# Kernel optimization log

Measured on AMD Instinct MI355X. Metric: run time of the kernel, lower is better.

## Reference

```python
import jax, jax.numpy as jnp
import numpy as np

B, N, C, D, H, L, F = 64, 256, 16, 512, 8, 8, 2048
HD = D // H
PI = np.pi


def _ln(x, w, b, eps=1e-5):
    mu = jnp.mean(x, -1, keepdims=True)
    var = jnp.mean(jnp.square(x - mu), -1, keepdims=True)
    return (x - mu) * jax.lax.rsqrt(var + eps) * w + b


def _forward(x_node, x_full, Wp, bp, cls, e_w1, e_b1, e_w2, e_b2, edge_scale,
             qkv_w, qkv_b, out_w, out_b, ln1_w, ln1_b, ln2_w, ln2_b,
             ff1_w, ff1_b, ff2_w, ff2_b, cl_ln_w, cl_ln_b, cl_w1, cl_b1, cl_w2, cl_b2):
    Bq, Nq, _ = x_node.shape
    # pairwise kaon geometry from absolute y/phi
    y = x_full[:, :, 14]
    phi = x_full[:, :, 15]
    dy = jnp.abs(y[:, :, None] - y[:, None, :])                                  # [B,N,N]
    dphi = jnp.abs(jnp.mod(phi[:, :, None] - phi[:, None, :] + PI, 2 * PI) - PI)
    dr = jnp.sqrt(dy * dy + dphi * dphi + 1e-8)
    ef = jnp.stack([dy, dphi, dr], -1)                                           # [B,N,N,3]
    hmid = jax.nn.gelu(ef @ e_w1.T + e_b1, approximate=False)                    # [B,N,N,16]
    raw = hmid @ e_w2.T + e_b2                                                   # [B,N,N,H]
    central = jnp.mean(raw, axis=2).transpose(0, 2, 1)                           # [B,H,N]
    edge_bias = raw.transpose(0, 3, 1, 2)                                        # [B,H,N,N]
    bias = jnp.zeros((Bq, H, Nq + 1, Nq + 1), x_node.dtype)
    bias = bias.at[:, :, 1:, 1:].set(edge_bias)
    bias = bias.at[:, :, 0, 1:].set(central * edge_scale)
    bias = bias.at[:, :, 1:, 0].set(central * edge_scale)

    h = x_node @ Wp.T + bp
    h = jnp.concatenate([jnp.broadcast_to(cls, (Bq, 1, D)), h], axis=1)          # [B,S,D]
    S = Nq + 1
    scale = 1.0 / np.sqrt(HD)
    for l in range(L):  # pre-norm TransformerEncoderLayer (activation=relu, no final norm)
        x = _ln(h, ln1_w[l], ln1_b[l])
        qkv = x @ qkv_w[l].T + qkv_b[l]
        q, k, v = jnp.split(qkv, 3, axis=-1)
        q = q.reshape(Bq, S, H, HD).transpose(0, 2, 1, 3)
        k = k.reshape(Bq, S, H, HD).transpose(0, 2, 1, 3)
        v = v.reshape(Bq, S, H, HD).transpose(0, 2, 1, 3)
        scores = jnp.einsum('bhqd,bhkd->bhqk', q, k) * scale + bias
        attn = jax.nn.softmax(scores, axis=-1)
        o = jnp.einsum('bhqk,bhkd->bhqd', attn, v).transpose(0, 2, 1, 3).reshape(Bq, S, D)
        h = h + o @ out_w[l].T + out_b[l]
        x = _ln(h, ln2_w[l], ln2_b[l])
        h = h + jax.nn.relu(x @ ff1_w[l].T + ff1_b[l]) @ ff2_w[l].T + ff2_b[l]
    x = _ln(h[:, 0], cl_ln_w, cl_ln_b)
    return jax.nn.gelu(x @ cl_w1.T + cl_b1, approximate=False) @ cl_w2.T + cl_b2  # [B,2]


def setup_inputs() -> dict:
    key = jax.random.key(0)
    ks = iter(jax.random.split(key, 40))
    f32 = jnp.float32

    def nrm(shape, s=0.02):
        return (s * jax.random.normal(next(ks), shape)).astype(f32)

    return {
        'x_node': jax.random.normal(next(ks), (B, N, C), f32),
        'x_full': jax.random.normal(next(ks), (B, N, 16), f32),
        'Wp': nrm((D, C)), 'bp': jnp.zeros((D,), f32),
        'cls': nrm((1, 1, D)),
        'e_w1': nrm((16, 3), 0.3), 'e_b1': jnp.zeros((16,), f32),
        'e_w2': nrm((H, 16), 0.01), 'e_b2': jnp.zeros((H,), f32),
        'edge_scale': jnp.full((1,), 0.1, f32),
        'qkv_w': nrm((L, 3 * D, D)), 'qkv_b': jnp.zeros((L, 3 * D), f32),
        'out_w': nrm((L, D, D)), 'out_b': jnp.zeros((L, D), f32),
        'ln1_w': jnp.ones((L, D), f32), 'ln1_b': jnp.zeros((L, D), f32),
        'ln2_w': jnp.ones((L, D), f32), 'ln2_b': jnp.zeros((L, D), f32),
        'ff1_w': nrm((L, F, D)), 'ff1_b': jnp.zeros((L, F), f32),
        'ff2_w': nrm((L, D, F)), 'ff2_b': jnp.zeros((L, D), f32),
        'cl_ln_w': jnp.ones((D,), f32), 'cl_ln_b': jnp.zeros((D,), f32),
        'cl_w1': nrm((D // 2, D)), 'cl_b1': jnp.zeros((D // 2,), f32),
        'cl_w2': nrm((2, D // 2)), 'cl_b2': jnp.zeros((2,), f32),
    }


def reference(x_node, x_full, Wp, bp, cls, e_w1, e_b1, e_w2, e_b2, edge_scale,
              qkv_w, qkv_b, out_w, out_b, ln1_w, ln1_b, ln2_w, ln2_b,
              ff1_w, ff1_b, ff2_w, ff2_b, cl_ln_w, cl_ln_b, cl_w1, cl_b1, cl_w2, cl_b2):
    return _forward(x_node, x_full, Wp, bp, cls, e_w1, e_b1, e_w2, e_b2, edge_scale,
                    qkv_w, qkv_b, out_w, out_b, ln1_w, ln1_b, ln2_w, ln2_b,
                    ff1_w, ff1_b, ff2_w, ff2_b, cl_ln_w, cl_ln_b, cl_w1, cl_b1, cl_w2, cl_b2)
```

## Files before the change

kernel.cpp:

```cpp
#include <hip/hip_runtime.h>
#include <hip/hip_bf16.h>
#include <stdint.h>

#define PI_F     3.14159265358979323846f
#define TWO_PI_F 6.28318530717958647692f
#define INV2PI_F 0.15915494309189535f

typedef __attribute__((ext_vector_type(8))) short bf16x8;
typedef __attribute__((ext_vector_type(4))) float f32x4;

#define BB 64
#define NN 256
#define SS 257
#define DD 512
#define HH 8
#define HDD 64
#define LL 8
#define MTOK 16448
#define MPAD 16512
#define BSTR 264
#define VSTR 320

__device__ __forceinline__ float b2f(unsigned short u){
  union { float f; uint32_t i; } c; c.i = ((uint32_t)u) << 16; return c.f;
}
__device__ __forceinline__ unsigned short f2b(float f){
  union { float f; uint32_t i; } c; c.f = f;
  uint32_t r = c.i + 0x7FFFu + ((c.i >> 16) & 1u);
  return (unsigned short)(r >> 16);
}
__device__ __forceinline__ float gelu_fast(float z){
  const float z2 = z*z;
  const float u2 = z * (1.5957691216f + 0.071354816f*z2);
  const float e = __expf(u2);
  const float th = 1.f - 2.f/(1.f + e);
  return 0.5f*z*(1.f + th);
}

typedef __attribute__((address_space(1))) unsigned char ga_t;
typedef __attribute__((address_space(3))) unsigned char ls_t;
__device__ __forceinline__ void gl_lds16(const void* g, void* l){
  __builtin_amdgcn_global_load_lds((ga_t*)g, (ls_t*)l, 16, 0, 0);
}

__global__ __launch_bounds__(256) void cvt_kernel(const float* __restrict__ src,
                                                  unsigned short* __restrict__ dst, int n2){
  int i = blockIdx.x*256 + threadIdx.x;
  int stride = gridDim.x*256;
  for (; i < n2; i += stride){
    float2 v = ((const float2*)src)[i];
    ((uint32_t*)dst)[i] = (uint32_t)f2b(v.x) | ((uint32_t)f2b(v.y) << 16);
  }
}

__global__ __launch_bounds__(256) void edge_kernel(
    const float* __restrict__ x_full, const float* __restrict__ e_w1, const float* __restrict__ e_b1,
    const float* __restrict__ e_w2, const float* __restrict__ e_b2,
    unsigned short* __restrict__ bias, float* __restrict__ central)
{
  const int bi = blockIdx.x;
  const int b = bi >> 8, i = bi & 255;
  const int j = threadIdx.x;
  const float yi = x_full[((long)b*NN + i)*16 + 14];
  const float fi = x_full[((long)b*NN + i)*16 + 15];
  const float yj = x_full[((long)b*NN + j)*16 + 14];
  const float fj = x_full[((long)b*NN + j)*16 + 15];
  const float dy = fabsf(yi - yj);
  const float xw = fi - fj + PI_F;
  const float tw = xw * INV2PI_F;
  const float md = (tw - floorf(tw)) * TWO_PI_F;
  const float dphi = fabsf(md - PI_F);
  const float dr = sqrtf(dy*dy + dphi*dphi + 1e-8f);
  float raw[8];
  #pragma unroll
  for (int hh = 0; hh < 8; ++hh) raw[hh] = e_b2[hh];
  #pragma unroll
  for (int k = 0; k < 16; ++k){
    float z = e_w1[k*3]*dy + e_w1[k*3+1]*dphi + e_w1[k*3+2]*dr + e_b1[k];
    float g = gelu_fast(z);
    #pragma unroll
    for (int hh = 0; hh < 8; ++hh) raw[hh] += g * e_w2[hh*16 + k];
  }
  #pragma unroll
  for (int hh = 0; hh < 8; ++hh)
    bias[(((long)b*HH + hh)*SS + 1 + i)*BSTR + 1 + j] = f2b(raw[hh]);
  #pragma unroll
  for (int m = 1; m < 64; m <<= 1)
    #pragma unroll
    for (int hh = 0; hh < 8; ++hh) raw[hh] += __shfl_xor(raw[hh], m);
  __shared__ float cw[4][8];
  const int wv = j >> 6;
  if ((j & 63) == 0)
    for (int hh = 0; hh < 8; ++hh) cw[wv][hh] = raw[hh];
  __syncthreads();
  if (j < 8){
    float t = cw[0][j] + cw[1][j] + cw[2][j] + cw[3][j];
    central[((long)b*NN + i)*HH + j] = t * (1.f/NN);
  }
}

__global__ __launch_bounds__(256) void edge_border_kernel(
    const float* __restrict__ central, const float* __restrict__ edge_scale,
    unsigned short* __restrict__ bias)
{
  const int bh = blockIdx.x;
  const int b = bh >> 3, h = bh & 7;
  const int j = threadIdx.x;
  const float es = edge_scale[0];
  const float cv = central[((long)b*NN + j)*HH + h] * es;
  const long base = (long)bh*SS*BSTR;
  const unsigned short u = f2b(cv);
  bias[base + 1 + j] = u;
  bias[base + (long)(1+j)*BSTR] = u;
  if (j == 0) bias[base] = 0;
}

__global__ __launch_bounds__(256) void proj_kernel(
    const float* __restrict__ x_node, const float* __restrict__ Wp,
    const float* __restrict__ bp, const float* __restrict__ cls, float* __restrict__ hb)
{
  const int t = blockIdx.x;
  const int tid = threadIdx.x;
  const int b = t / SS, s2 = t - b*SS;
  float2 o;
  if (s2 == 0){
    o = *(const float2*)(cls + tid*2);
  } else {
    const float* xr = x_node + ((long)b*NN + (s2-1))*16;
    float xv[16];
    #pragma unroll
    for (int c2 = 0; c2 < 16; ++c2) xv[c2] = xr[c2];
    float oo[2];
    #pragma unroll
    for (int e = 0; e < 2; ++e){
      int d = tid*2 + e;
      float a = bp[d];
      const float* wr2 = Wp + (long)d*16;
      #pragma unroll
      for (int c2 = 0; c2 < 16; ++c2) a += xv[c2]*wr2[c2];
      oo[e] = a;
    }
    o.x = oo[0]; o.y = oo[1];
  }
  *(float2*)(hb + (long)t*DD + tid*2) = o;
}

__global__ __launch_bounds__(256) void ln_kernel(
    const float* __restrict__ hb, const float* __restrict__ w,
    const float* __restrict__ bbv, unsigned short* __restrict__ xb)
{
  const int tok = blockIdx.x*4 + (threadIdx.x >> 6);
  const int lane = threadIdx.x & 63;
  const float4* p = (const float4*)(hb + (long)tok*DD + lane*8);
  const float4 a = p[0], bq = p[1];
  float s  = a.x + a.y + a.z + a.w + bq.x + bq.y + bq.z + bq.w;
  float ss = a.x*a.x + a.y*a.y + a.z*a.z + a.w*a.w
           + bq.x*bq.x + bq.y*bq.y + bq.z*bq.z + bq.w*bq.w;
  #pragma unroll
  for (int m = 1; m < 64; m <<= 1){ s += __shfl_xor(s, m); ss += __shfl_xor(ss, m); }
  const float mu = s * (1.f/DD);
  const float var = ss * (1.f/DD) - mu*mu;
  const float rs = rsqrtf(var + 1e-5f);
  const float4* wp = (const float4*)(w + lane*8);
  const float4* bp2 = (const float4*)(bbv + lane*8);
  const float4 w0 = wp[0], w1 = wp[1];
  const float4 b0 = bp2[0], b1 = bp2[1];
  bf16x8 o;
  o[0] = (short)f2b((a.x - mu)*rs*w0.x + b0.x);
  o[1] = (short)f2b((a.y - mu)*rs*w0.y + b0.y);
  o[2] = (short)f2b((a.z - mu)*rs*w0.z + b0.z);
  o[3] = (short)f2b((a.w - mu)*rs*w0.w + b0.w);
  o[4] = (short)f2b((bq.x - mu)*rs*w1.x + b1.x);
  o[5] = (short)f2b((bq.y - mu)*rs*w1.y + b1.y);
  o[6] = (short)f2b((bq.z - mu)*rs*w1.z + b1.z);
  o[7] = (short)f2b((bq.w - mu)*rs*w1.w + b1.w);
  *(bf16x8*)(xb + (long)tok*DD + lane*8) = o;
}

template<int EPI, int MI, int NI, int WPE>
__global__ __launch_bounds__(256, WPE) void gemm_kernel(
    const unsigned short* __restrict__ A, const unsigned short* __restrict__ Bw,
    const float* __restrict__ bias, void* __restrict__ Cout,
    int M, int N, int K, int ldc, int nblocks)
{
  __shared__ unsigned short As[MI*32*64];
  __shared__ unsigned short Bs[NI*32*64];
  const int tid = threadIdx.x;
  const int lane = tid & 63;
  const int wave = tid >> 6;
  const int wr = wave >> 1, wc = wave & 1;
  const int l16 = lane & 15, lhi = lane >> 4;

  const int nwg = gridDim.x;
  const int q8 = nwg >> 3, r8 = nwg & 7;
  const int xcd = blockIdx.x & 7, idx = blockIdx.x >> 3;
  const int lin = (xcd < r8 ? xcd*(q8+1) : r8*(q8+1) + (xcd-r8)*q8) + idx;
  const int mb = lin / nblocks;
  const int nb = lin - mb*nblocks;
  const long m0 = (long)mb * (MI*32);
  const long n0 = (long)nb * (NI*32);

  f32x4 acc[MI][NI];
  const f32x4 z4 = {0.f, 0.f, 0.f, 0.f};
  #pragma unroll
  for (int mi = 0; mi < MI; ++mi)
    #pragma unroll
    for (int ni = 0; ni < NI; ++ni) acc[mi][ni] = z4;

  const char* Ab = (const char*)A;
  const char* Bb = (const char*)Bw;
  const int nkt = K >> 6;
  for (int kt = 0; kt < nkt; ++kt){
    #pragma unroll
    for (int c = 0; c < MI; ++c){
      const int bo = c*4096 + tid*16;
      const int row = bo >> 7;
      const int kb = bo & 127;
      gl_lds16(Ab + ((m0+row)*(long)K)*2 + (long)kt*128 + kb, (char*)As + bo);
    }
    #pragma unroll
    for (int c = 0; c < NI; ++c){
      const int bo = c*4096 + tid*16;
      const int row = bo >> 7;
      const int kb = bo & 127;
      gl_lds16(Bb + ((n0+row)*(long)K)*2 + (long)kt*128 + kb, (char*)Bs + bo);
    }
    __syncthreads();
    #pragma unroll
    for (int kd = 0; kd < 2; ++kd){
      bf16x8 af[MI], bfr[NI];
      #pragma unroll
      for (int mi = 0; mi < MI; ++mi)
        af[mi] = *(const bf16x8*)((const char*)As + (wr*(MI*16) + mi*16 + l16)*128 + kd*64 + lhi*16);
      #pragma unroll
      for (int ni = 0; ni < NI; ++ni)
        bfr[ni] = *(const bf16x8*)((const char*)Bs + (wc*(NI*16) + ni*16 + l16)*128 + kd*64 + lhi*16);
      #pragma unroll
      for (int mi = 0; mi < MI; ++mi)
        #pragma unroll
        for (int ni = 0; ni < NI; ++ni)
          acc[mi][ni] = __builtin_amdgcn_mfma_f32_16x16x32_bf16(af[mi], bfr[ni], acc[mi][ni], 0, 0, 0);
    }
    __syncthreads();
  }
  #pragma unroll
  for (int mi = 0; mi < MI; ++mi){
    #pragma unroll
    for (int ni = 0; ni < NI; ++ni){
      const int col = (int)n0 + wc*(NI*16) + ni*16 + l16;
      const float bn = bias[col];
      const int rowb = (int)m0 + wr*(MI*16) + mi*16 + lhi*4;
      #pragma unroll
      for (int r = 0; r < 4; ++r){
        const int m = rowb + r;
        if (m < M){
          float v = acc[mi][ni][r] + bn;
          if (EPI == 1) v = fmaxf(v, 0.f);
          if (EPI == 2) ((float*)Cout)[(long)m*ldc + col] += v;
          else          ((unsigned short*)Cout)[(long)m*ldc + col] = f2b(v);
        }
      }
    }
  }
}

__global__ __launch_bounds__(256) void vtrans_kernel(
    const unsigned short* __restrict__ qkv, unsigned short* __restrict__ vt)
{
  const int bh = blockIdx.x;
  const int c = blockIdx.y;
  const int b = bh >> 3, h = bh & 7;
  __shared__ unsigned short tile[64][72];
  const int tid = threadIdx.x;
  const int rr = tid >> 3, ch = tid & 7;
  #pragma unroll
  for (int it = 0; it < 2; ++it){
    const int sl = it*32 + rr;
    const long tok = (long)b*SS + c*64 + sl;
    bf16x8 v = *(const bf16x8*)(qkv + tok*1536 + 1024 + h*64 + ch*8);
    *(bf16x8*)(&tile[sl][ch*8]) = v;
  }
  __syncthreads();
  #pragma unroll
  for (int it = 0; it < 2; ++it){
    const int d = it*32 + rr;
    const int s0 = c*64 + ch*8;
    bf16x8 o;
    #pragma unroll
    for (int e = 0; e < 8; ++e){
      const int sgl = s0 + e;
      o[e] = (sgl < SS) ? (short)tile[ch*8 + e][d] : (short)0;
    }
    *(bf16x8*)(vt + ((long)bh*HDD + d)*VSTR + s0) = o;
  }
}

__global__ __launch_bounds__(576) void flash_kernel(
    const unsigned short* __restrict__ qkv, const unsigned short* __restrict__ vt,
    const unsigned short* __restrict__ bias, unsigned short* __restrict__ ob)
{
  const int bh = blockIdx.x;
  const int b = bh >> 3, h = bh & 7;
  const int qt = threadIdx.x >> 6;
  const int lane = threadIdx.x & 63;
  const int l16 = lane & 15, lhi = lane >> 4;

  __shared__ unsigned short Ks[2][2048];
  __shared__ unsigned short Vs[2][2048];
  __shared__ unsigned short Bsh[9][2][1024];
  __shared__ unsigned short pt[9][1024];
  unsigned short* ptw = pt[qt];

  bf16x8 qf[2][2];
  #pragma unroll
  for (int mi = 0; mi < 2; ++mi)
    #pragma unroll
    for (int kd = 0; kd < 2; ++kd){
      const long tok = (long)b*SS + qt*32 + mi*16 + l16;
      qf[mi][kd] = *(const bf16x8*)(qkv + tok*1536 + h*64 + kd*32 + lhi*8);
    }

  auto stage = [&](int jtn, int bb){
    const int rB = lane >> 2, cB = lane & 3;
    const char* gb = (const char*)bias + (((long)bh*SS + qt*32)*BSTR + (long)jtn*32)*2;
    char* lb = (char*)&Bsh[qt][bb][0];
    gl_lds16(gb + (long)rB*BSTR*2        + cB*16, lb + lane*16);
    gl_lds16(gb + (long)(16+rB)*BSTR*2   + cB*16, lb + 1024 + lane*16);
    if (qt < 4){
      const int rK = lane >> 3, cK = lane & 7;
      gl_lds16((const char*)qkv + (((long)b*SS + jtn*32 + qt*8 + rK)*1536 + 512 + h*64)*2 + ((cK ^ rK)*16),
               (char*)&Ks[bb][0] + qt*1024 + lane*16);
    } else if (qt < 8){
      const int rV = lane >> 2, cV = lane & 3;
      const int d = (qt-4)*16 + rV;
      gl_lds16((const char*)vt + (((long)bh*64 + d)*VSTR + (long)jtn*32)*2 + ((cV ^ (rV & 3))*16),
               (char*)&Vs[bb][0] + (qt-4)*1024 + lane*16);
    }
  };

  f32x4 oacc[2][4];
  const f32x4 z4 = {0.f, 0.f, 0.f, 0.f};
  #pragma unroll
  for (int mi = 0; mi < 2; ++mi)
    #pragma unroll
    for (int ni = 0; ni < 4; ++ni) oacc[mi][ni] = z4;
  float mrow[2][4], lrow[2][4];
  #pragma unroll
  for (int mi = 0; mi < 2; ++mi)
    #pragma unroll
    for (int r = 0; r < 4; ++r){ mrow[mi][r] = -1e30f; lrow[mi][r] = 0.f; }

  stage(0, 0);
  __builtin_amdgcn_sched_barrier(0);

  for (int jt = 0; jt < 9; ++jt){
    const int cur = jt & 1;
    if (jt < 8){
      stage(jt+1, cur ^ 1);
      __builtin_amdgcn_sched_barrier(0);
      if (qt < 8) asm volatile("s_waitcnt vmcnt(3)" ::: "memory");
      else        asm volatile("s_waitcnt vmcnt(2)" ::: "memory");
    } else {
      asm volatile("s_waitcnt vmcnt(0)" ::: "memory");
    }
    __builtin_amdgcn_sched_barrier(0);
    __builtin_amdgcn_s_barrier();
    __builtin_amdgcn_sched_barrier(0);

    bf16x8 kf[2][2];
    #pragma unroll
    for (int ni = 0; ni < 2; ++ni)
      #pragma unroll
      for (int kd = 0; kd < 2; ++kd){
        const int row = ni*16 + l16;
        const int sw = (kd*4 + lhi) ^ (row & 7);
        kf[ni][kd] = *(const bf16x8*)((const char*)&Ks[cur][0] + row*128 + sw*16);
      }
    f32x4 sacc[2][2];
    #pragma unroll
    for (int mi = 0; mi < 2; ++mi)
      #pragma unroll
      for (int ni = 0; ni < 2; ++ni) sacc[mi][ni] = z4;
    __builtin_amdgcn_s_setprio(1);
    #pragma unroll
    for (int kd = 0; kd < 2; ++kd)
      #pragma unroll
      for (int mi = 0; mi < 2; ++mi)
        #pragma unroll
        for (int ni = 0; ni < 2; ++ni)
          sacc[mi][ni] = __builtin_amdgcn_mfma_f32_16x16x32_bf16(qf[mi][kd], kf[ni][kd], sacc[mi][ni], 0, 0, 0);
    __builtin_amdgcn_s_setprio(0);

    float sv[2][2][4];
    #pragma unroll
    for (int mi = 0; mi < 2; ++mi)
      #pragma unroll
      for (int ni = 0; ni < 2; ++ni)
        #pragma unroll
        for (int r = 0; r < 4; ++r){
          const int col = jt*32 + ni*16 + l16;
          float x = sacc[mi][ni][r] * 0.125f;
          x += b2f(Bsh[qt][cur][(mi*16 + lhi*4 + r)*32 + ni*16 + l16]);
          if (col >= SS) x = -1e30f;
          sv[mi][ni][r] = x;
        }
    #pragma unroll
    for (int mi = 0; mi < 2; ++mi)
      #pragma unroll
      for (int r = 0; r < 4; ++r){
        float pm = fmaxf(sv[mi][0][r], sv[mi][1][r]);
        #pragma unroll
        for (int sh = 1; sh < 16; sh <<= 1) pm = fmaxf(pm, __shfl_xor(pm, sh));
        const float mold = mrow[mi][r];
        const float mnew = fmaxf(mold, pm);
        const float corr = __expf(mold - mnew);
        mrow[mi][r] = mnew;
        float psum = 0.f;
        #pragma unroll
        for (int ni = 0; ni < 2; ++ni){
          const float p = __expf(sv[mi][ni][r] - mnew);
          sv[mi][ni][r] = p;
          psum += p;
        }
        #pragma unroll
        for (int sh = 1; sh < 16; sh <<= 1) psum += __shfl_xor(psum, sh);
        lrow[mi][r] = lrow[mi][r]*corr + psum;
        #pragma unroll
        for (int ni = 0; ni < 4; ++ni) oacc[mi][ni][r] = oacc[mi][ni][r]*corr;
      }
    #pragma unroll
    for (int mi = 0; mi < 2; ++mi)
      #pragma unroll
      for (int ni = 0; ni < 2; ++ni)
        #pragma unroll
        for (int r = 0; r < 4; ++r)
          ptw[(mi*16 + lhi*4 + r)*32 + ni*16 + l16] = f2b(sv[mi][ni][r]);
    bf16x8 pf[2];
    #pragma unroll
    for (int mi = 0; mi < 2; ++mi)
      pf[mi] = *(const bf16x8*)(ptw + (mi*16 + l16)*32 + lhi*8);
    bf16x8 vf[4];
    #pragma unroll
    for (int ni = 0; ni < 4; ++ni){
      const int d = ni*16 + l16;
      const int sw = lhi ^ (d & 3);
      vf[ni] = *(const bf16x8*)((const char*)&Vs[cur][0] + d*64 + sw*16);
    }
    __builtin_amdgcn_s_setprio(1);
    #pragma unroll
    for (int mi = 0; mi < 2; ++mi)
      #pragma unroll
      for (int ni = 0; ni < 4; ++ni)
        oacc[mi][ni] = __builtin_amdgcn_mfma_f32_16x16x32_bf16(pf[mi], vf[ni], oacc[mi][ni], 0, 0, 0);
    __builtin_amdgcn_s_setprio(0);

    __builtin_amdgcn_sched_barrier(0);
    __builtin_amdgcn_s_barrier();
    __builtin_amdgcn_sched_barrier(0);
  }

  #pragma unroll
  for (int mi = 0; mi < 2; ++mi)
    #pragma unroll
    for (int r = 0; r < 4; ++r){
      const int row = qt*32 + mi*16 + lhi*4 + r;
      if (row < SS){
        const float inv = 1.0f / lrow[mi][r];
        const long tok = (long)b*SS + row;
        #pragma unroll
        for (int ni = 0; ni < 4; ++ni)
          ob[tok*DD + h*HDD + ni*16 + l16] = f2b(oacc[mi][ni][r] * inv);
      }
    }
}

__global__ __launch_bounds__(256) void cls_kernel(
    const float* __restrict__ hb, const float* __restrict__ lw, const float* __restrict__ lb,
    const float* __restrict__ w1, const float* __restrict__ b1,
    const float* __restrict__ w2, const float* __restrict__ b2, float* __restrict__ out)
{
  const int b = blockIdx.x;
  const int tid = threadIdx.x;
  const float* row = hb + (long)b*SS*DD;
  const float2 v = *(const float2*)(row + tid*2);
  float s = v.x + v.y, ss = v.x*v.x + v.y*v.y;
  #pragma unroll
  for (int m = 1; m < 64; m <<= 1){ s += __shfl_xor(s, m); ss += __shfl_xor(ss, m); }
  __shared__ float red[8];
  const int wv = tid >> 6;
  if ((tid & 63) == 0){ red[wv] = s; red[4+wv] = ss; }
  __syncthreads();
  s  = red[0]+red[1]+red[2]+red[3];
  ss = red[4]+red[5]+red[6]+red[7];
  const float mu = s * (1.f/DD);
  const float var = ss * (1.f/DD) - mu*mu;
  const float rs = rsqrtf(var + 1e-5f);
  __shared__ __align__(16) float xs[DD];
  xs[tid*2]   = (v.x - mu)*rs*lw[tid*2]   + lb[tid*2];
  xs[tid*2+1] = (v.y - mu)*rs*lw[tid*2+1] + lb[tid*2+1];
  __syncthreads();
  float a = b1[tid];
  const float4* w1v = (const float4*)(w1 + (long)tid*DD);
  const float4* xsv = (const float4*)xs;
  for (int d4 = 0; d4 < DD/4; ++d4){
    const float4 wv4 = w1v[d4], xv4 = xsv[d4];
    a += wv4.x*xv4.x + wv4.y*xv4.y + wv4.z*xv4.z + wv4.w*xv4.w;
  }
  const float g = 0.5f*a*(1.f + erff(a*0.70710678118f));
  float p0 = g * w2[tid];
  float p1 = g * w2[256 + tid];
  #pragma unroll
  for (int m = 1; m < 64; m <<= 1){ p0 += __shfl_xor(p0, m); p1 += __shfl_xor(p1, m); }
  __shared__ float r2[8];
  if ((tid & 63) == 0){ r2[wv] = p0; r2[4+wv] = p1; }
  __syncthreads();
  if (tid == 0) out[b*2]   = r2[0]+r2[1]+r2[2]+r2[3] + b2[0];
  if (tid == 1) out[b*2+1] = r2[4]+r2[5]+r2[6]+r2[7] + b2[1];
}

extern "C" void kernel_launch(void* const* d_in, const int* in_sizes, int n_in,
                              void* d_out, int out_size, void* d_ws, size_t ws_size,
                              hipStream_t stream) {
  const float* x_node    = (const float*)d_in[0];
  const float* x_full    = (const float*)d_in[1];
  const float* Wp        = (const float*)d_in[2];
  const float* bp        = (const float*)d_in[3];
  const float* cls       = (const float*)d_in[4];
  const float* e_w1      = (const float*)d_in[5];
  const float* e_b1      = (const float*)d_in[6];
  const float* e_w2      = (const float*)d_in[7];
  const float* e_b2      = (const float*)d_in[8];
  const float* edge_scale= (const float*)d_in[9];
  const float* qkv_w     = (const float*)d_in[10];
  const float* qkv_b     = (const float*)d_in[11];
  const float* out_w     = (const float*)d_in[12];
  const float* out_b     = (const float*)d_in[13];
  const float* ln1_w     = (const float*)d_in[14];
  const float* ln1_b     = (const float*)d_in[15];
  const float* ln2_w     = (const float*)d_in[16];
  const float* ln2_b     = (const float*)d_in[17];
  const float* ff1_w     = (const float*)d_in[18];
  const float* ff1_b     = (const float*)d_in[19];
  const float* ff2_w     = (const float*)d_in[20];
  const float* ff2_b     = (const float*)d_in[21];
  const float* cl_ln_w   = (const float*)d_in[22];
  const float* cl_ln_b   = (const float*)d_in[23];
  const float* cl_w1     = (const float*)d_in[24];
  const float* cl_b1     = (const float*)d_in[25];
  const float* cl_w2     = (const float*)d_in[26];
  const float* cl_b2     = (const float*)d_in[27];
  float* out = (float*)d_out;

  char* w = (char*)d_ws;
  size_t off = 0;
  auto take = [&](size_t bytes)->char*{
    char* p = w + off;
    off += (bytes + 255) & ~(size_t)255;
    return p;
  };
  unsigned short* wq8   = (unsigned short*)take((size_t)LL*1536*512*2);
  unsigned short* wo8   = (unsigned short*)take((size_t)LL*512*512*2);
  unsigned short* wf1   = (unsigned short*)take((size_t)LL*2048*512*2);
  unsigned short* wf2   = (unsigned short*)take((size_t)LL*512*2048*2);
  unsigned short* bias16= (unsigned short*)take((size_t)BB*HH*SS*BSTR*2 + 65536);
  float*          cent  = (float*)take((size_t)BB*NN*HH*4);
  float*          hbuf  = (float*)take((size_t)MPAD*DD*4);
  unsigned short* xb    = (unsigned short*)take((size_t)MPAD*DD*2);
  unsigned short* obuf  = (unsigned short*)take((size_t)MPAD*DD*2);
  unsigned short* qkvb  = (unsigned short*)take((size_t)MPAD*1536*2);
  unsigned short* vtb   = (unsigned short*)take((size_t)BB*HH*HDD*VSTR*2);
  unsigned short* ffb   = qkvb;

  cvt_kernel<<<4096, 256, 0, stream>>>(qkv_w, wq8, LL*1536*512/2);
  cvt_kernel<<<4096, 256, 0, stream>>>(out_w, wo8, LL*512*512/2);
  cvt_kernel<<<4096, 256, 0, stream>>>(ff1_w, wf1, LL*2048*512/2);
  cvt_kernel<<<4096, 256, 0, stream>>>(ff2_w, wf2, LL*512*2048/2);

  edge_kernel<<<dim3(BB*NN), 256, 0, stream>>>(x_full, e_w1, e_b1, e_w2, e_b2, bias16, cent);
  edge_border_kernel<<<dim3(BB*HH), 256, 0, stream>>>(cent, edge_scale, bias16);
  proj_kernel<<<dim3(MTOK), 256, 0, stream>>>(x_node, Wp, bp, cls, hbuf);

  for (int l = 0; l < LL; ++l){
    ln_kernel<<<dim3(MTOK/4), 256, 0, stream>>>(hbuf, ln1_w + l*DD, ln1_b + l*DD, xb);
    gemm_kernel<0,4,4,4><<<dim3(129*12), 256, 0, stream>>>(xb, wq8 + (size_t)l*1536*512,
        qkv_b + (size_t)l*1536, qkvb, MTOK, 1536, 512, 1536, 12);
    vtrans_kernel<<<dim3(512, 5), 256, 0, stream>>>(qkvb, vtb);
    flash_kernel<<<dim3(512), 576, 0, stream>>>(qkvb, vtb, bias16, obuf);
    gemm_kernel<2,2,2,6><<<dim3(257*8), 256, 0, stream>>>(obuf, wo8 + (size_t)l*512*512,
        out_b + (size_t)l*DD, hbuf, MTOK, 512, 512, 512, 8);
    ln_kernel<<<dim3(MTOK/4), 256, 0, stream>>>(hbuf, ln2_w + l*DD, ln2_b + l*DD, xb);
    gemm_kernel<1,4,4,4><<<dim3(129*16), 256, 0, stream>>>(xb, wf1 + (size_t)l*2048*512,
        ff1_b + (size_t)l*2048, ffb, MTOK, 2048, 512, 2048, 16);
    gemm_kernel<2,2,2,6><<<dim3(257*8), 256, 0, stream>>>(ffb, wf2 + (size_t)l*512*2048,
        ff2_b + (size_t)l*DD, hbuf, MTOK, 512, 2048, 512, 8);
  }
  cls_kernel<<<dim3(BB), 256, 0, stream>>>(hbuf, cl_ln_w, cl_ln_b, cl_w1, cl_b1, cl_w2, cl_b2, out);
}
```

Baseline: 2.623 ms.

## Stage residual-add GEMM epilogue through LDS with float4 stores and taller tiles

The residual-add GEMM epilogue (out-proj and FF2) now writes accumulators into shared memory in two halves, then does coalesced float4 read-modify-write of the fp32 residual with the bias added. This replaces scattered 4-byte strided accesses. Those two GEMMs also switch from 64x64 to 128x64 tiles, which halves the grid and raises reuse of the B operand per workgroup. The GELU divide is replaced by a hardware reciprocal. The costs are extra LDS traffic, extra barriers, and fewer workgroups, which may hurt occupancy.

```diff
diff --git a/kernel.cpp b/kernel.cpp
--- a/kernel.cpp
+++ b/kernel.cpp
@@ -33,7 +33,8 @@
   const float z2 = z*z;
   const float u2 = z * (1.5957691216f + 0.071354816f*z2);
   const float e = __expf(u2);
-  const float th = 1.f - 2.f/(1.f + e);
+  const float r = __builtin_amdgcn_rcpf(1.f + e);
+  const float th = 1.f - 2.f*r;
   return 0.5f*z*(1.f + th);
 }
 
@@ -183,8 +184,9 @@
     const float* __restrict__ bias, void* __restrict__ Cout,
     int M, int N, int K, int ldc, int nblocks)
 {
-  __shared__ unsigned short As[MI*32*64];
-  __shared__ unsigned short Bs[NI*32*64];
+  __shared__ __align__(16) char smem[MI*4096 + NI*4096];
+  unsigned short* As = (unsigned short*)smem;
+  unsigned short* Bs = (unsigned short*)(smem + MI*4096);
   const int tid = threadIdx.x;
   const int lane = tid & 63;
   const int wave = tid >> 6;
@@ -243,21 +245,60 @@
     }
     __syncthreads();
   }
-  #pragma unroll
-  for (int mi = 0; mi < MI; ++mi){
-    #pragma unroll
-    for (int ni = 0; ni < NI; ++ni){
-      const int col = (int)n0 + wc*(NI*16) + ni*16 + l16;
-      const float bn = bias[col];
-      const int rowb = (int)m0 + wr*(MI*16) + mi*16 + lhi*4;
-      #pragma unroll
-      for (int r = 0; r < 4; ++r){
-        const int m = rowb + r;
-        if (m < M){
-          float v = acc[mi][ni][r] + bn;
-          if (EPI == 1) v = fmaxf(v, 0.f);
-          if (EPI == 2) ((float*)Cout)[(long)m*ldc + col] += v;
-          else          ((unsigned short*)Cout)[(long)m*ldc + col] = f2b(v);
+
+  if (EPI == 2){
+    float* Cs = (float*)smem;
+    const int NC = NI*32;
+    const int LDSC = NC + 4;
+    float* Cg = (float*)Cout;
+    #pragma unroll
+    for (int half = 0; half < 2; ++half){
+      if (wr == half){
+        #pragma unroll
+        for (int mi = 0; mi < MI; ++mi)
+          #pragma unroll
+          for (int ni = 0; ni < NI; ++ni){
+            const int col = wc*(NI*16) + ni*16 + l16;
+            #pragma unroll
+            for (int r = 0; r < 4; ++r)
+              Cs[(mi*16 + lhi*4 + r)*LDSC + col] = acc[mi][ni][r];
+          }
+      }
+      __syncthreads();
+      #pragma unroll
+      for (int it = 0; it < MI; ++it){
+        const int idx = tid + it*256;
+        const int c4 = idx & 15;
+        const int row = idx >> 4;
+        const int gm = (int)m0 + half*(MI*16) + row;
+        if (gm < M){
+          const long go = (long)gm*ldc + n0 + c4*4;
+          float4 cv = *(float4*)&Cg[go];
+          const float* ls = &Cs[row*LDSC + c4*4];
+          const float4 bv = *(const float4*)&bias[n0 + c4*4];
+          cv.x += ls[0] + bv.x; cv.y += ls[1] + bv.y;
+          cv.z += ls[2] + bv.z; cv.w += ls[3] + bv.w;
+          *(float4*)&Cg[go] = cv;
+        }
+      }
+      __syncthreads();
+    }
+  } else {
+    #pragma unroll
+    for (int mi = 0; mi < MI; ++mi){
+      #pragma unroll
+      for (int ni = 0; ni < NI; ++ni){
+        const int col = (int)n0 + wc*(NI*16) + ni*16 + l16;
+        const float bn = bias[col];
+        const int rowb = (int)m0 + wr*(MI*16) + mi*16 + lhi*4;
+        #pragma unroll
+        for (int r = 0; r < 4; ++r){
+          const int m = rowb + r;
+          if (m < M){
+            float v = acc[mi][ni][r] + bn;
+            if (EPI == 1) v = fmaxf(v, 0.f);
+            ((unsigned short*)Cout)[(long)m*ldc + col] = f2b(v);
+          }
         }
       }
     }
@@ -586,12 +627,12 @@
         qkv_b + (size_t)l*1536, qkvb, MTOK, 1536, 512, 1536, 12);
     vtrans_kernel<<<dim3(512, 5), 256, 0, stream>>>(qkvb, vtb);
     flash_kernel<<<dim3(512), 576, 0, stream>>>(qkvb, vtb, bias16, obuf);
-    gemm_kernel<2,2,2,6><<<dim3(257*8), 256, 0, stream>>>(obuf, wo8 + (size_t)l*512*512,
+    gemm_kernel<2,4,2,6><<<dim3(129*8), 256, 0, stream>>>(obuf, wo8 + (size_t)l*512*512,
         out_b + (size_t)l*DD, hbuf, MTOK, 512, 512, 512, 8);
     ln_kernel<<<dim3(MTOK/4), 256, 0, stream>>>(hbuf, ln2_w + l*DD, ln2_b + l*DD, xb);
     gemm_kernel<1,4,4,4><<<dim3(129*16), 256, 0, stream>>>(xb, wf1 + (size_t)l*2048*512,
         ff1_b + (size_t)l*2048, ffb, MTOK, 2048, 512, 2048, 16);
-    gemm_kernel<2,2,2,6><<<dim3(257*8), 256, 0, stream>>>(ffb, wf2 + (size_t)l*512*2048,
+    gemm_kernel<2,4,2,6><<<dim3(129*8), 256, 0, stream>>>(ffb, wf2 + (size_t)l*512*2048,
         ff2_b + (size_t)l*DD, hbuf, MTOK, 512, 2048, 512, 8);
   }
   cls_kernel<<<dim3(BB), 256, 0, stream>>>(hbuf, cl_ln_w, cl_ln_b, cl_w1, cl_b1, cl_w2, cl_b2, out);
```

New measurement: 2.530 ms, median of 2. -3.5%, faster.
